# Kernel tuning notes

Hardware: AMD Instinct MI355X
Metric: run time of the kernel (lower is better)

## Reference

```python
import jax, jax.numpy as jnp
import numpy as np

B, N, H = 8, 2048, 256


def setup_inputs() -> dict:
    key = jax.random.key(0)
    ks = jax.random.split(key, 8)
    s = 1.0 / np.sqrt(H)
    return {
        "node": jax.random.normal(ks[0], (B, N, H), dtype=jnp.float32),
        "graph": jax.random.uniform(ks[1], (B, N, N), dtype=jnp.float32),
        "W1": jax.random.normal(ks[2], (H, H), dtype=jnp.float32) * s,
        "b1": jnp.zeros((H,), dtype=jnp.float32),
        "W2": jax.random.normal(ks[3], (H, H), dtype=jnp.float32) * s,
        "b2": jnp.zeros((H,), dtype=jnp.float32),
        "Wout": jax.random.normal(ks[4], (H, 2 * H), dtype=jnp.float32) * (1.0 / np.sqrt(2 * H)),
        "bout": jnp.zeros((H,), dtype=jnp.float32),
    }


def reference(node, graph, W1, b1, W2, b2, Wout, bout):
    # Symmetric normalization D^{-1/2} A D^{-1/2}, batched and vectorized
    # (equivalent to the per-sample diag-mm loop in the original).
    d = jnp.sum(graph, axis=2)                # [B, N] row sums (torch sum(1) on [N,N])
    dinv = d ** -0.5                          # [B, N]
    g = graph * dinv[:, :, None] * dinv[:, None, :]  # [B, N, N]

    # node_info = relu(fc1(g @ node)); fc2(g @ node_info)
    h = jax.nn.relu(jnp.einsum("bnm,bmh->bnh", g, node) @ W1.T + b1)
    h = jax.nn.relu(jnp.einsum("bnm,bmh->bnh", g, h) @ W2.T + b2)

    agg = jnp.concatenate([node, h], axis=2)  # [B, N, 2H]
    return jax.nn.relu(agg @ Wout.T + bout)   # [B, N, H]
```

## Files before the change

### kernel.cpp

```cpp
#include <hip/hip_runtime.h>
#include <stdint.h>

typedef __attribute__((ext_vector_type(4))) float f32x4;
typedef __attribute__((ext_vector_type(8))) short bf16x8;

static __device__ __forceinline__ unsigned short f2bf(float x) {
  unsigned int u = __builtin_bit_cast(unsigned int, x);
  u = (u + 0x7fffu + ((u >> 16) & 1u)) >> 16;
  return (unsigned short)u;
}

#define GLD16(g, l)                                                            \
  __builtin_amdgcn_global_load_lds(                                            \
      (__attribute__((address_space(1))) const void*)(g),                      \
      (__attribute__((address_space(3))) void*)(l), 16, 0, 0)

__global__ __launch_bounds__(256) void rowscale_cvt_k(
    const float* __restrict__ g, float* __restrict__ dinv,
    unsigned short* __restrict__ gb, const float* __restrict__ W1,
    const float* __restrict__ W2, const float* __restrict__ Wout,
    unsigned short* __restrict__ wb) {
  if (blockIdx.x >= 4096) {
    int base = (blockIdx.x - 4096) * 2048;
#pragma unroll
    for (int i = 0; i < 8; ++i) {
      int idx = base + i * 256 + threadIdx.x;
      float v;
      if (idx < 65536) v = W1[idx];
      else if (idx < 131072) v = W2[idx - 65536];
      else v = Wout[idx - 131072];
      wb[idx] = f2bf(v);
    }
    return;
  }
  int row = blockIdx.x * 4 + (threadIdx.x >> 6);
  int lane = threadIdx.x & 63;
  const float* p = g + (long)row * 2048;
  float4 v[8];
  float s = 0.f;
#pragma unroll
  for (int i = 0; i < 8; ++i) {
    v[i] = *(const float4*)(p + (lane + i * 64) * 4);
    s += v[i].x + v[i].y + v[i].z + v[i].w;
  }
#pragma unroll
  for (int off = 32; off; off >>= 1) s += __shfl_xor(s, off, 64);
  float di = rsqrtf(s);
  if (lane == 0) dinv[row] = di;
  unsigned short* q = gb + (long)row * 2048;
#pragma unroll
  for (int i = 0; i < 8; ++i) {
    ushort4 u;
    u.x = f2bf(v[i].x * di); u.y = f2bf(v[i].y * di);
    u.z = f2bf(v[i].z * di); u.w = f2bf(v[i].w * di);
    *(ushort4*)(q + (lane + i * 64) * 4) = u;
  }
}

__global__ __launch_bounds__(256) void prep_node_k(
    const float* __restrict__ node, const float* __restrict__ dinv,
    unsigned short* __restrict__ nodeT, unsigned short* __restrict__ agg) {
  __shared__ unsigned short t[64 * 68];
  int tid = threadIdx.x;
  int m0 = blockIdx.x * 64, h0 = blockIdx.y * 64;
  long b = blockIdx.z;
#pragma unroll
  for (int i = 0; i < 4; ++i) {
    int idx = tid + 256 * i;
    int r = idx >> 4, c4 = idx & 15;
    long m = m0 + r;
    float4 v = *(const float4*)(node + (b * 2048 + m) * 256 + h0 + c4 * 4);
    float di = dinv[b * 2048 + m];
    ushort4 u;
    u.x = f2bf(v.x); u.y = f2bf(v.y); u.z = f2bf(v.z); u.w = f2bf(v.w);
    *(ushort4*)(agg + (b * 2048 + m) * 512 + h0 + c4 * 4) = u;
    t[(c4 * 4 + 0) * 68 + r] = f2bf(v.x * di);
    t[(c4 * 4 + 1) * 68 + r] = f2bf(v.y * di);
    t[(c4 * 4 + 2) * 68 + r] = f2bf(v.z * di);
    t[(c4 * 4 + 3) * 68 + r] = f2bf(v.w * di);
  }
  __syncthreads();
#pragma unroll
  for (int i = 0; i < 4; ++i) {
    int idx = tid + 256 * i;
    int hr = idx >> 4, c4 = idx & 15;
    ushort4 o = *(const ushort4*)(&t[hr * 68 + c4 * 4]);
    *(ushort4*)(nodeT + (b * 256 + h0 + hr) * 2048 + m0 + c4 * 4) = o;
  }
}

template <bool TRANS_OUT>
__global__ __launch_bounds__(512, 1) void mega_k(
    const unsigned short* __restrict__ A, const unsigned short* __restrict__ Bt,
    const unsigned short* __restrict__ W, const float* __restrict__ bias,
    const float* __restrict__ dinv, unsigned short* __restrict__ Cout,
    long bBatch) {
  __shared__ char lds[81920];
  char* ldsA = lds;
  char* ldsB = lds + 16384;
  char* ldsX = lds;
  char* ldsW = lds + 32768;

  int tid = threadIdx.x;
  int lane = tid & 63;
  int w = tid >> 6;
  int wm = w >> 2, wn = w & 3;

  int bid = blockIdx.x;
  int batch = bid & 7;
  int mt = bid >> 3;
  long row0 = ((long)batch * 32 + mt) * 64;
  const unsigned short* Bb = Bt + (long)batch * bBatch;

  f32x4 acc[2][4] = {};

  auto stageA = [&](int kt, int buf) {
    int r = tid >> 3, j = tid & 7;
    int jg = j ^ (r & 7);
    GLD16(A + (row0 + r) * 2048 + kt * 64 + jg * 8,
          ldsA + buf * 8192 + w * 1024);
  };
  auto stageB = [&](int kt, int buf) {
#pragma unroll
    for (int i = 0; i < 4; ++i) {
      int slot = i * 512 + tid;
      int c = slot >> 3, j = slot & 7;
      int jg = j ^ (c & 7);
      GLD16(Bb + (long)c * 2048 + kt * 64 + jg * 8,
            ldsB + buf * 32768 + (i * 8 + w) * 1024);
    }
  };
  auto compute1 = [&](int buf) {
    char* bA = ldsA + buf * 8192;
    char* bB = ldsB + buf * 32768;
    bf16x8 a[2][2], bb[4][2];
#pragma unroll
    for (int m = 0; m < 2; ++m)
#pragma unroll
      for (int kk = 0; kk < 2; ++kk) {
        int row = wm * 32 + m * 16 + (lane & 15);
        int off = (row * 128 + kk * 64 + (lane >> 4) * 16) ^ ((row & 7) << 4);
        a[m][kk] = *(const bf16x8*)(bA + off);
      }
#pragma unroll
    for (int n = 0; n < 4; ++n)
#pragma unroll
      for (int kk = 0; kk < 2; ++kk) {
        int col = wn * 64 + n * 16 + (lane & 15);
        int off = (col * 128 + kk * 64 + (lane >> 4) * 16) ^ ((col & 7) << 4);
        bb[n][kk] = *(const bf16x8*)(bB + off);
      }
#pragma unroll
    for (int m = 0; m < 2; ++m)
#pragma unroll
      for (int n = 0; n < 4; ++n) {
        acc[m][n] = __builtin_amdgcn_mfma_f32_16x16x32_bf16(a[m][0], bb[n][0],
                                                            acc[m][n], 0, 0, 0);
        acc[m][n] = __builtin_amdgcn_mfma_f32_16x16x32_bf16(a[m][1], bb[n][1],
                                                            acc[m][n], 0, 0, 0);
      }
  };

  stageA(0, 0);
  stageB(0, 0);
  __syncthreads();
  int cur = 0;
  for (int t = 0; t < 32; ++t) {
    int nxt = cur ^ 1;
    if (t + 1 < 32) {
      stageA(t + 1, nxt);
      stageB(t + 1, nxt);
    }
    compute1(cur);
    __syncthreads();
    cur = nxt;
  }
  __syncthreads();

#pragma unroll
  for (int m = 0; m < 2; ++m)
#pragma unroll
    for (int n = 0; n < 4; ++n) {
      int col = wn * 64 + n * 16 + (lane & 15);
#pragma unroll
      for (int r = 0; r < 4; ++r) {
        int row = wm * 32 + m * 16 + (lane >> 4) * 4 + r;
        int off = (row * 512 + col * 2) ^ ((row & 7) << 4);
        *(unsigned short*)(ldsX + off) = f2bf(acc[m][n][r]);
      }
    }

  f32x4 acc2[2][4] = {};
  for (int kt = 0; kt < 4; ++kt) {
    __syncthreads();
#pragma unroll
    for (int i = 0; i < 4; ++i) {
      int slot = i * 512 + tid;
      int c = slot >> 3, j = slot & 7;
      int jg = j ^ (c & 7);
      GLD16(W + (long)c * 256 + kt * 64 + jg * 8, ldsW + (i * 8 + w) * 1024);
    }
    __syncthreads();
    bf16x8 a[2][2], bb[4][2];
#pragma unroll
    for (int m = 0; m < 2; ++m)
#pragma unroll
      for (int kk = 0; kk < 2; ++kk) {
        int row = wm * 32 + m * 16 + (lane & 15);
        int off = (row * 512 + kt * 128 + kk * 64 + (lane >> 4) * 16) ^
                  ((row & 7) << 4);
        a[m][kk] = *(const bf16x8*)(ldsX + off);
      }
#pragma unroll
    for (int n = 0; n < 4; ++n)
#pragma unroll
      for (int kk = 0; kk < 2; ++kk) {
        int col = wn * 64 + n * 16 + (lane & 15);
        int off = (col * 128 + kk * 64 + (lane >> 4) * 16) ^ ((col & 7) << 4);
        bb[n][kk] = *(const bf16x8*)(ldsW + off);
      }
#pragma unroll
    for (int m = 0; m < 2; ++m)
#pragma unroll
      for (int n = 0; n < 4; ++n) {
        acc2[m][n] = __builtin_amdgcn_mfma_f32_16x16x32_bf16(a[m][0], bb[n][0],
                                                             acc2[m][n], 0, 0, 0);
        acc2[m][n] = __builtin_amdgcn_mfma_f32_16x16x32_bf16(a[m][1], bb[n][1],
                                                             acc2[m][n], 0, 0, 0);
      }
  }

  if (TRANS_OUT) {
    __syncthreads();
    unsigned short* tb = (unsigned short*)lds;
#pragma unroll
    for (int m = 0; m < 2; ++m)
#pragma unroll
      for (int n = 0; n < 4; ++n) {
        int col = wn * 64 + n * 16 + (lane & 15);
        float bv = bias[col];
#pragma unroll
        for (int r = 0; r < 4; ++r) {
          int rl = wm * 32 + m * 16 + (lane >> 4) * 4 + r;
          float v = fmaxf(acc2[m][n][r] + bv, 0.f) * dinv[row0 + rl];
          tb[col * 72 + rl] = f2bf(v);
        }
      }
    __syncthreads();
    int rin = (int)(row0 & 2047);
#pragma unroll
    for (int i = 0; i < 4; ++i) {
      int id = i * 512 + tid;
      int col = id >> 3, seg = id & 7;
      bf16x8 u = *(const bf16x8*)(tb + col * 72 + seg * 8);
      *(bf16x8*)(Cout + ((long)batch * 256 + col) * 2048 + rin + seg * 8) = u;
    }
  } else {
#pragma unroll
    for (int m = 0; m < 2; ++m)
#pragma unroll
      for (int n = 0; n < 4; ++n) {
        int col = wn * 64 + n * 16 + (lane & 15);
        float bv = bias[col];
#pragma unroll
        for (int r = 0; r < 4; ++r) {
          long row = row0 + wm * 32 + m * 16 + (lane >> 4) * 4 + r;
          float v = fmaxf(acc2[m][n][r] + bv, 0.f);
          Cout[row * 512 + col] = f2bf(v);
        }
      }
  }
}

__global__ __launch_bounds__(256, 2) void gemm_f3(
    const unsigned short* __restrict__ A, const unsigned short* __restrict__ Bt,
    const float* __restrict__ bias, float* __restrict__ C) {
  __shared__ char lds[65536];
  char* ldsA = lds;
  char* ldsB = lds + 32768;
  int tid = threadIdx.x;
  int lane = tid & 63;
  int w = tid >> 6;
  int wm = w >> 1, wn = w & 1;

  int bid = blockIdx.x;
  int gt = ((bid & 7) << 5) + (bid >> 3);
  int mt = gt >> 1;
  int col0 = (gt & 1) * 128;
  long row0 = (long)mt * 128;

  f32x4 acc[4][4] = {};
  auto stageA = [&](int kt, int buf) {
#pragma unroll
    for (int i = 0; i < 4; ++i) {
      int slot = i * 256 + tid;
      int r = slot >> 3, j = slot & 7;
      int jg = j ^ (r & 7);
      GLD16(A + (row0 + r) * 512 + kt * 64 + jg * 8,
            ldsA + buf * 16384 + (i * 4 + w) * 1024);
    }
  };
  auto stageB = [&](int kt, int buf) {
#pragma unroll
    for (int i = 0; i < 4; ++i) {
      int slot = i * 256 + tid;
      int c = slot >> 3, j = slot & 7;
      int jg = j ^ (c & 7);
      GLD16(Bt + (long)(col0 + c) * 512 + kt * 64 + jg * 8,
            ldsB + buf * 16384 + (i * 4 + w) * 1024);
    }
  };
  auto compute = [&](int buf) {
    char* bA = ldsA + buf * 16384;
    char* bB = ldsB + buf * 16384;
    bf16x8 a[4][2], bb[4][2];
#pragma unroll
    for (int m = 0; m < 4; ++m)
#pragma unroll
      for (int kk = 0; kk < 2; ++kk) {
        int row = wm * 64 + m * 16 + (lane & 15);
        int off = (row * 128 + kk * 64 + (lane >> 4) * 16) ^ ((row & 7) << 4);
        a[m][kk] = *(const bf16x8*)(bA + off);
      }
#pragma unroll
    for (int n = 0; n < 4; ++n)
#pragma unroll
      for (int kk = 0; kk < 2; ++kk) {
        int col = wn * 64 + n * 16 + (lane & 15);
        int off = (col * 128 + kk * 64 + (lane >> 4) * 16) ^ ((col & 7) << 4);
        bb[n][kk] = *(const bf16x8*)(bB + off);
      }
#pragma unroll
    for (int m = 0; m < 4; ++m)
#pragma unroll
      for (int n = 0; n < 4; ++n) {
        acc[m][n] = __builtin_amdgcn_mfma_f32_16x16x32_bf16(a[m][0], bb[n][0],
                                                            acc[m][n], 0, 0, 0);
        acc[m][n] = __builtin_amdgcn_mfma_f32_16x16x32_bf16(a[m][1], bb[n][1],
                                                            acc[m][n], 0, 0, 0);
      }
  };

  stageA(0, 0);
  stageB(0, 0);
  __syncthreads();
  int cur = 0;
  for (int t = 0; t < 8; ++t) {
    int nxt = cur ^ 1;
    if (t + 1 < 8) {
      stageA(t + 1, nxt);
      stageB(t + 1, nxt);
    }
    compute(cur);
    __syncthreads();
    cur = nxt;
  }
#pragma unroll
  for (int m = 0; m < 4; ++m)
#pragma unroll
    for (int n = 0; n < 4; ++n) {
      int col = col0 + wn * 64 + n * 16 + (lane & 15);
      float bv = bias[col & 255];
#pragma unroll
      for (int r = 0; r < 4; ++r) {
        long row = row0 + wm * 64 + m * 16 + (lane >> 4) * 4 + r;
        C[row * 256 + (col & 255)] = fmaxf(acc[m][n][r] + bv, 0.f);
      }
    }
}

extern "C" void kernel_launch(void* const* d_in, const int* in_sizes, int n_in,
                              void* d_out, int out_size, void* d_ws,
                              size_t ws_size, hipStream_t stream) {
  const float* node = (const float*)d_in[0];
  const float* graph = (const float*)d_in[1];
  const float* W1 = (const float*)d_in[2];
  const float* b1 = (const float*)d_in[3];
  const float* W2 = (const float*)d_in[4];
  const float* b2 = (const float*)d_in[5];
  const float* Wout = (const float*)d_in[6];
  const float* bout = (const float*)d_in[7];
  float* out = (float*)d_out;

  char* p = (char*)d_ws;
  float* dinv = (float*)p;                    p += 16384 * 4;
  unsigned short* wb = (unsigned short*)p;    p += 262144 * 2;
  unsigned short* gb = (unsigned short*)p;    p += 8L * 2048 * 2048 * 2;
  unsigned short* nodeT = (unsigned short*)p; p += 8L * 256 * 2048 * 2;
  unsigned short* xT = (unsigned short*)p;    p += 8L * 256 * 2048 * 2;
  unsigned short* agg = (unsigned short*)p;   p += 8L * 2048 * 512 * 2;

  rowscale_cvt_k<<<4224, 256, 0, stream>>>(graph, dinv, gb, W1, W2, Wout, wb);
  prep_node_k<<<dim3(32, 4, 8), 256, 0, stream>>>(node, dinv, nodeT, agg);
  mega_k<true><<<256, 512, 0, stream>>>(gb, nodeT, wb, b1, dinv, xT,
                                        256L * 2048);
  mega_k<false><<<256, 512, 0, stream>>>(gb, xT, wb + 65536, b2, dinv,
                                         agg + 256, 256L * 2048);
  gemm_f3<<<256, 256, 0, stream>>>(agg, wb + 131072, bout, out);
}
```

Before: 310.4 us.

## Fuse final output GEMM into second graph layer and triple-buffer main loop

Merges the second graph-aggregation/fc2 kernel with the final concat+Wout GEMM, so h stays in LDS and only a bf16 copy of node is read back instead of writing and rereading the agg buffer. It also changes the 32-step main K loop from double to triple buffering, using explicit vmcnt waits and a raw barrier so loads run two tiles ahead. LDS per block grows to 120KB. The final GEMM now runs on 64-row tiles with reloaded Wout slices, which lowers its data reuse compared with the old 128x128 gemm_f3.

```diff
diff --git a/kernel.cpp b/kernel.cpp
--- a/kernel.cpp
+++ b/kernel.cpp
@@ -59,7 +59,7 @@
 
 __global__ __launch_bounds__(256) void prep_node_k(
     const float* __restrict__ node, const float* __restrict__ dinv,
-    unsigned short* __restrict__ nodeT, unsigned short* __restrict__ agg) {
+    unsigned short* __restrict__ nodeT, unsigned short* __restrict__ nodeB) {
   __shared__ unsigned short t[64 * 68];
   int tid = threadIdx.x;
   int m0 = blockIdx.x * 64, h0 = blockIdx.y * 64;
@@ -73,7 +73,7 @@
     float di = dinv[b * 2048 + m];
     ushort4 u;
     u.x = f2bf(v.x); u.y = f2bf(v.y); u.z = f2bf(v.z); u.w = f2bf(v.w);
-    *(ushort4*)(agg + (b * 2048 + m) * 512 + h0 + c4 * 4) = u;
+    *(ushort4*)(nodeB + (b * 2048 + m) * 256 + h0 + c4 * 4) = u;
     t[(c4 * 4 + 0) * 68 + r] = f2bf(v.x * di);
     t[(c4 * 4 + 1) * 68 + r] = f2bf(v.y * di);
     t[(c4 * 4 + 2) * 68 + r] = f2bf(v.z * di);
@@ -89,18 +89,14 @@
   }
 }
 
-template <bool TRANS_OUT>
-__global__ __launch_bounds__(512, 1) void mega_k(
+#define LDS_BYTES 122880
+#define B_RING 24576
+
+__global__ __launch_bounds__(512, 1) void mega1_k(
     const unsigned short* __restrict__ A, const unsigned short* __restrict__ Bt,
     const unsigned short* __restrict__ W, const float* __restrict__ bias,
-    const float* __restrict__ dinv, unsigned short* __restrict__ Cout,
-    long bBatch) {
-  __shared__ char lds[81920];
-  char* ldsA = lds;
-  char* ldsB = lds + 16384;
-  char* ldsX = lds;
-  char* ldsW = lds + 32768;
-
+    const float* __restrict__ dinv, unsigned short* __restrict__ Cout) {
+  __shared__ char lds[LDS_BYTES];
   int tid = threadIdx.x;
   int lane = tid & 63;
   int w = tid >> 6;
@@ -110,15 +106,14 @@
   int batch = bid & 7;
   int mt = bid >> 3;
   long row0 = ((long)batch * 32 + mt) * 64;
-  const unsigned short* Bb = Bt + (long)batch * bBatch;
+  const unsigned short* Bb = Bt + (long)batch * (256L * 2048);
 
   f32x4 acc[2][4] = {};
 
   auto stageA = [&](int kt, int buf) {
     int r = tid >> 3, j = tid & 7;
     int jg = j ^ (r & 7);
-    GLD16(A + (row0 + r) * 2048 + kt * 64 + jg * 8,
-          ldsA + buf * 8192 + w * 1024);
+    GLD16(A + (row0 + r) * 2048 + kt * 64 + jg * 8, lds + buf * 8192 + w * 1024);
   };
   auto stageB = [&](int kt, int buf) {
 #pragma unroll
@@ -127,12 +122,12 @@
       int c = slot >> 3, j = slot & 7;
       int jg = j ^ (c & 7);
       GLD16(Bb + (long)c * 2048 + kt * 64 + jg * 8,
-            ldsB + buf * 32768 + (i * 8 + w) * 1024);
+            lds + B_RING + buf * 32768 + (i * 8 + w) * 1024);
     }
   };
   auto compute1 = [&](int buf) {
-    char* bA = ldsA + buf * 8192;
-    char* bB = ldsB + buf * 32768;
+    char* bA = lds + buf * 8192;
+    char* bB = lds + B_RING + buf * 32768;
     bf16x8 a[2][2], bb[4][2];
 #pragma unroll
     for (int m = 0; m < 2; ++m)
@@ -161,22 +156,24 @@
       }
   };
 
-  stageA(0, 0);
-  stageB(0, 0);
-  __syncthreads();
-  int cur = 0;
+  stageA(0, 0); stageB(0, 0);
+  stageA(1, 1); stageB(1, 1);
   for (int t = 0; t < 32; ++t) {
-    int nxt = cur ^ 1;
-    if (t + 1 < 32) {
-      stageA(t + 1, nxt);
-      stageB(t + 1, nxt);
-    }
-    compute1(cur);
-    __syncthreads();
-    cur = nxt;
-  }
-  __syncthreads();
-
+    if (t < 31) asm volatile("s_waitcnt vmcnt(5)" ::: "memory");
+    else        asm volatile("s_waitcnt vmcnt(0)" ::: "memory");
+    __builtin_amdgcn_s_barrier();
+    if (t + 2 < 32) {
+      int nb = (t + 2) % 3;
+      stageA(t + 2, nb);
+      stageB(t + 2, nb);
+    }
+    compute1(t % 3);
+  }
+  asm volatile("s_waitcnt vmcnt(0)" ::: "memory");
+  __syncthreads();
+
+  char* ldsX = lds;
+  char* ldsW = lds + 32768;
 #pragma unroll
   for (int m = 0; m < 2; ++m)
 #pragma unroll
@@ -230,95 +227,75 @@
       }
   }
 
-  if (TRANS_OUT) {
-    __syncthreads();
-    unsigned short* tb = (unsigned short*)lds;
-#pragma unroll
-    for (int m = 0; m < 2; ++m)
-#pragma unroll
-      for (int n = 0; n < 4; ++n) {
-        int col = wn * 64 + n * 16 + (lane & 15);
-        float bv = bias[col];
-#pragma unroll
-        for (int r = 0; r < 4; ++r) {
-          int rl = wm * 32 + m * 16 + (lane >> 4) * 4 + r;
-          float v = fmaxf(acc2[m][n][r] + bv, 0.f) * dinv[row0 + rl];
-          tb[col * 72 + rl] = f2bf(v);
-        }
-      }
-    __syncthreads();
-    int rin = (int)(row0 & 2047);
-#pragma unroll
-    for (int i = 0; i < 4; ++i) {
-      int id = i * 512 + tid;
-      int col = id >> 3, seg = id & 7;
-      bf16x8 u = *(const bf16x8*)(tb + col * 72 + seg * 8);
-      *(bf16x8*)(Cout + ((long)batch * 256 + col) * 2048 + rin + seg * 8) = u;
-    }
-  } else {
-#pragma unroll
-    for (int m = 0; m < 2; ++m)
-#pragma unroll
-      for (int n = 0; n < 4; ++n) {
-        int col = wn * 64 + n * 16 + (lane & 15);
-        float bv = bias[col];
-#pragma unroll
-        for (int r = 0; r < 4; ++r) {
-          long row = row0 + wm * 32 + m * 16 + (lane >> 4) * 4 + r;
-          float v = fmaxf(acc2[m][n][r] + bv, 0.f);
-          Cout[row * 512 + col] = f2bf(v);
-        }
-      }
-  }
-}
-
-__global__ __launch_bounds__(256, 2) void gemm_f3(
+  __syncthreads();
+  unsigned short* tb = (unsigned short*)lds;
+#pragma unroll
+  for (int m = 0; m < 2; ++m)
+#pragma unroll
+    for (int n = 0; n < 4; ++n) {
+      int col = wn * 64 + n * 16 + (lane & 15);
+      float bv = bias[col];
+#pragma unroll
+      for (int r = 0; r < 4; ++r) {
+        int rl = wm * 32 + m * 16 + (lane >> 4) * 4 + r;
+        float v = fmaxf(acc2[m][n][r] + bv, 0.f) * dinv[row0 + rl];
+        tb[col * 72 + rl] = f2bf(v);
+      }
+    }
+  __syncthreads();
+  int rin = (int)(row0 & 2047);
+#pragma unroll
+  for (int i = 0; i < 4; ++i) {
+    int id = i * 512 + tid;
+    int col = id >> 3, seg = id & 7;
+    bf16x8 u = *(const bf16x8*)(tb + col * 72 + seg * 8);
+    *(bf16x8*)(Cout + ((long)batch * 256 + col) * 2048 + rin + seg * 8) = u;
+  }
+}
+
+__global__ __launch_bounds__(512, 1) void mega2f3_k(
     const unsigned short* __restrict__ A, const unsigned short* __restrict__ Bt,
-    const float* __restrict__ bias, float* __restrict__ C) {
-  __shared__ char lds[65536];
-  char* ldsA = lds;
-  char* ldsB = lds + 32768;
+    const unsigned short* __restrict__ W2b, const float* __restrict__ b2,
+    const unsigned short* __restrict__ nodeB, const unsigned short* __restrict__ Wo,
+    const float* __restrict__ bout, float* __restrict__ out) {
+  __shared__ char lds[LDS_BYTES];
   int tid = threadIdx.x;
   int lane = tid & 63;
   int w = tid >> 6;
-  int wm = w >> 1, wn = w & 1;
+  int wm = w >> 2, wn = w & 3;
 
   int bid = blockIdx.x;
-  int gt = ((bid & 7) << 5) + (bid >> 3);
-  int mt = gt >> 1;
-  int col0 = (gt & 1) * 128;
-  long row0 = (long)mt * 128;
-
-  f32x4 acc[4][4] = {};
+  int batch = bid & 7;
+  int mt = bid >> 3;
+  long row0 = ((long)batch * 32 + mt) * 64;
+  const unsigned short* Bb = Bt + (long)batch * (256L * 2048);
+
+  f32x4 acc[2][4] = {};
+
   auto stageA = [&](int kt, int buf) {
+    int r = tid >> 3, j = tid & 7;
+    int jg = j ^ (r & 7);
+    GLD16(A + (row0 + r) * 2048 + kt * 64 + jg * 8, lds + buf * 8192 + w * 1024);
+  };
+  auto stageB = [&](int kt, int buf) {
 #pragma unroll
     for (int i = 0; i < 4; ++i) {
-      int slot = i * 256 + tid;
-      int r = slot >> 3, j = slot & 7;
-      int jg = j ^ (r & 7);
-      GLD16(A + (row0 + r) * 512 + kt * 64 + jg * 8,
-            ldsA + buf * 16384 + (i * 4 + w) * 1024);
-    }
-  };
-  auto stageB = [&](int kt, int buf) {
-#pragma unroll
-    for (int i = 0; i < 4; ++i) {
-      int slot = i * 256 + tid;
+      int slot = i * 512 + tid;
       int c = slot >> 3, j = slot & 7;
       int jg = j ^ (c & 7);
-      GLD16(Bt + (long)(col0 + c) * 512 + kt * 64 + jg * 8,
-            ldsB + buf * 16384 + (i * 4 + w) * 1024);
-    }
-  };
-  auto compute = [&](int buf) {
-    char* bA = ldsA + buf * 16384;
-    char* bB = ldsB + buf * 16384;
-    bf16x8 a[4][2], bb[4][2];
-#pragma unroll
-    for (int m = 0; m < 4; ++m)
-#pragma unroll
-      for (int kk = 0; kk < 2; ++kk) {
-        int row = wm * 64 + m * 16 + (lane & 15);
+      GLD16(Bb + (long)c * 2048 + kt * 64 + jg * 8,
+            lds + B_RING + buf * 32768 + (i * 8 + w) * 1024);
+    }
+  };
+  auto compute1 = [&](int buf) {
+    char* bA = lds + buf * 8192;
+    char* bB = lds + B_RING + buf * 32768;
+    bf16x8 a[2][2], bb[4][2];
+#pragma unroll
+    for (int m = 0; m < 2; ++m)
+#pragma unroll
+      for (int kk = 0; kk < 2; ++kk) {
+        int row = wm * 32 + m * 16 + (lane & 15);
         int off = (row * 128 + kk * 64 + (lane >> 4) * 16) ^ ((row & 7) << 4);
         a[m][kk] = *(const bf16x8*)(bA + off);
       }
@@ -331,7 +308,7 @@
         bb[n][kk] = *(const bf16x8*)(bB + off);
       }
 #pragma unroll
-    for (int m = 0; m < 4; ++m)
+    for (int m = 0; m < 2; ++m)
 #pragma unroll
       for (int n = 0; n < 4; ++n) {
         acc[m][n] = __builtin_amdgcn_mfma_f32_16x16x32_bf16(a[m][0], bb[n][0],
@@ -341,30 +318,154 @@
       }
   };
 
-  stageA(0, 0);
-  stageB(0, 0);
-  __syncthreads();
-  int cur = 0;
-  for (int t = 0; t < 8; ++t) {
-    int nxt = cur ^ 1;
-    if (t + 1 < 8) {
-      stageA(t + 1, nxt);
-      stageB(t + 1, nxt);
-    }
-    compute(cur);
-    __syncthreads();
-    cur = nxt;
-  }
-#pragma unroll
-  for (int m = 0; m < 4; ++m)
+  stageA(0, 0); stageB(0, 0);
+  stageA(1, 1); stageB(1, 1);
+  for (int t = 0; t < 32; ++t) {
+    if (t < 31) asm volatile("s_waitcnt vmcnt(5)" ::: "memory");
+    else        asm volatile("s_waitcnt vmcnt(0)" ::: "memory");
+    __builtin_amdgcn_s_barrier();
+    if (t + 2 < 32) {
+      int nb = (t + 2) % 3;
+      stageA(t + 2, nb);
+      stageB(t + 2, nb);
+    }
+    compute1(t % 3);
+  }
+  asm volatile("s_waitcnt vmcnt(0)" ::: "memory");
+  __syncthreads();
+
+  char* ldsX = lds;
+  char* ldsW = lds + 32768;
+#pragma unroll
+  for (int m = 0; m < 2; ++m)
 #pragma unroll
     for (int n = 0; n < 4; ++n) {
-      int col = col0 + wn * 64 + n * 16 + (lane & 15);
-      float bv = bias[col & 255];
+      int col = wn * 64 + n * 16 + (lane & 15);
 #pragma unroll
       for (int r = 0; r < 4; ++r) {
-        long row = row0 + wm * 64 + m * 16 + (lane >> 4) * 4 + r;
-        C[row * 256 + (col & 255)] = fmaxf(acc[m][n][r] + bv, 0.f);
+        int row = wm * 32 + m * 16 + (lane >> 4) * 4 + r;
+        int off = (row * 512 + col * 2) ^ ((row & 7) << 4);
+        *(unsigned short*)(ldsX + off) = f2bf(acc[m][n][r]);
+      }
+    }
+
+  f32x4 acc2[2][4] = {};
+  for (int kt = 0; kt < 4; ++kt) {
+    __syncthreads();
+#pragma unroll
+    for (int i = 0; i < 4; ++i) {
+      int slot = i * 512 + tid;
+      int c = slot >> 3, j = slot & 7;
+      int jg = j ^ (c & 7);
+      GLD16(W2b + (long)c * 256 + kt * 64 + jg * 8, ldsW + (i * 8 + w) * 1024);
+    }
+    __syncthreads();
+    bf16x8 a[2][2], bb[4][2];
+#pragma unroll
+    for (int m = 0; m < 2; ++m)
+#pragma unroll
+      for (int kk = 0; kk < 2; ++kk) {
+        int row = wm * 32 + m * 16 + (lane & 15);
+        int off = (row * 512 + kt * 128 + kk * 64 + (lane >> 4) * 16) ^
+                  ((row & 7) << 4);
+        a[m][kk] = *(const bf16x8*)(ldsX + off);
+      }
+#pragma unroll
+    for (int n = 0; n < 4; ++n)
+#pragma unroll
+      for (int kk = 0; kk < 2; ++kk) {
+        int col = wn * 64 + n * 16 + (lane & 15);
+        int off = (col * 128 + kk * 64 + (lane >> 4) * 16) ^ ((col & 7) << 4);
+        bb[n][kk] = *(const bf16x8*)(ldsW + off);
+      }
+#pragma unroll
+    for (int m = 0; m < 2; ++m)
+#pragma unroll
+      for (int n = 0; n < 4; ++n) {
+        acc2[m][n] = __builtin_amdgcn_mfma_f32_16x16x32_bf16(a[m][0], bb[n][0],
+                                                             acc2[m][n], 0, 0, 0);
+        acc2[m][n] = __builtin_amdgcn_mfma_f32_16x16x32_bf16(a[m][1], bb[n][1],
+                                                             acc2[m][n], 0, 0, 0);
+      }
+  }
+  __syncthreads();
+
+  char* Alo = lds;
+  char* Ahi = lds + 32768;
+  char* ldsW3 = lds + 65536;
+#pragma unroll
+  for (int m = 0; m < 2; ++m)
+#pragma unroll
+    for (int n = 0; n < 4; ++n) {
+      int col = wn * 64 + n * 16 + (lane & 15);
+      float bv = b2[col];
+#pragma unroll
+      for (int r = 0; r < 4; ++r) {
+        int row = wm * 32 + m * 16 + (lane >> 4) * 4 + r;
+        int off = (row * 512 + col * 2) ^ ((row & 7) << 4);
+        *(unsigned short*)(Ahi + off) = f2bf(fmaxf(acc2[m][n][r] + bv, 0.f));
+      }
+    }
+#pragma unroll
+  for (int i = 0; i < 4; ++i) {
+    int slot = i * 512 + tid;
+    int r = slot >> 5, j = slot & 31;
+    int jg = j ^ (r & 7);
+    GLD16(nodeB + (row0 + r) * 256 + jg * 8, Alo + (i * 8 + w) * 1024);
+  }
+
+  f32x4 acc3[2][4] = {};
+  for (int kt = 0; kt < 8; ++kt) {
+    __syncthreads();
+#pragma unroll
+    for (int i = 0; i < 4; ++i) {
+      int slot = i * 512 + tid;
+      int c = slot >> 3, j = slot & 7;
+      int jg = j ^ (c & 7);
+      GLD16(Wo + (long)c * 512 + kt * 64 + jg * 8, ldsW3 + (i * 8 + w) * 1024);
+    }
+    __syncthreads();
+    char* Asrc = (kt < 4) ? Alo : Ahi;
+    int ko = (kt & 3) * 128;
+    bf16x8 a[2][2], bb[4][2];
+#pragma unroll
+    for (int m = 0; m < 2; ++m)
+#pragma unroll
+      for (int kk = 0; kk < 2; ++kk) {
+        int row = wm * 32 + m * 16 + (lane & 15);
+        int off = (row * 512 + ko + kk * 64 + (lane >> 4) * 16) ^
+                  ((row & 7) << 4);
+        a[m][kk] = *(const bf16x8*)(Asrc + off);
+      }
+#pragma unroll
+    for (int n = 0; n < 4; ++n)
+#pragma unroll
+      for (int kk = 0; kk < 2; ++kk) {
+        int col = wn * 64 + n * 16 + (lane & 15);
+        int off = (col * 128 + kk * 64 + (lane >> 4) * 16) ^ ((col & 7) << 4);
+        bb[n][kk] = *(const bf16x8*)(ldsW3 + off);
+      }
+#pragma unroll
+    for (int m = 0; m < 2; ++m)
+#pragma unroll
+      for (int n = 0; n < 4; ++n) {
+        acc3[m][n] = __builtin_amdgcn_mfma_f32_16x16x32_bf16(a[m][0], bb[n][0],
+                                                             acc3[m][n], 0, 0, 0);
+        acc3[m][n] = __builtin_amdgcn_mfma_f32_16x16x32_bf16(a[m][1], bb[n][1],
+                                                             acc3[m][n], 0, 0, 0);
+      }
+  }
+
+#pragma unroll
+  for (int m = 0; m < 2; ++m)
+#pragma unroll
+    for (int n = 0; n < 4; ++n) {
+      int col = wn * 64 + n * 16 + (lane & 15);
+      float bv = bout[col];
+#pragma unroll
+      for (int r = 0; r < 4; ++r) {
+        long row = row0 + wm * 32 + m * 16 + (lane >> 4) * 4 + r;
+        out[row * 256 + col] = fmaxf(acc3[m][n][r] + bv, 0.f);
       }
     }
 }
@@ -388,13 +489,11 @@
   unsigned short* gb = (unsigned short*)p;    p += 8L * 2048 * 2048 * 2;
   unsigned short* nodeT = (unsigned short*)p; p += 8L * 256 * 2048 * 2;
   unsigned short* xT = (unsigned short*)p;    p += 8L * 256 * 2048 * 2;
-  unsigned short* agg = (unsigned short*)p;   p += 8L * 2048 * 512 * 2;
+  unsigned short* nodeB = (unsigned short*)p; p += 8L * 2048 * 256 * 2;
 
   rowscale_cvt_k<<<4224, 256, 0, stream>>>(graph, dinv, gb, W1, W2, Wout, wb);
-  prep_node_k<<<dim3(32, 4, 8), 256, 0, stream>>>(node, dinv, nodeT, agg);
-  mega_k<true><<<256, 512, 0, stream>>>(gb, nodeT, wb, b1, dinv, xT,
-                                        256L * 2048);
-  mega_k<false><<<256, 512, 0, stream>>>(gb, xT, wb + 65536, b2, dinv,
-                                         agg + 256, 256L * 2048);
-  gemm_f3<<<256, 256, 0, stream>>>(agg, wb + 131072, bout, out);
-}
+  prep_node_k<<<dim3(32, 4, 8), 256, 0, stream>>>(node, dinv, nodeT, nodeB);
+  mega1_k<<<256, 512, 0, stream>>>(gb, nodeT, wb, b1, dinv, xT);
+  mega2f3_k<<<256, 512, 0, stream>>>(gb, xT, wb + 65536, b2, nodeB,
+                                     wb + 131072, bout, out);
+}
```

Measured after the change: 296.5 us. 4.5% less time.
